# Kernel tuning notes

Hardware: AMD Instinct MI355X
Metric: run time of the kernel (lower is better)

The kernel has to match this reference:

```python
import jax, jax.numpy as jnp
import numpy as np

N_NODES = 50000
HEADS1 = 4
NEG_SLOPE = 0.2
EPS = 1e-16


def gat_conv(x, edge_index, W, att_src, att_dst, bias, heads, out_ch, concat):
    # edge_index: [2, E] with self-loops already appended by caller
    src, dst = edge_index[0], edge_index[1]
    N = x.shape[0]
    h = (x @ W).reshape(N, heads, out_ch)                      # [N, H, C]
    a_src = jnp.sum(h * att_src, axis=-1)                      # [N, H]
    a_dst = jnp.sum(h * att_dst, axis=-1)                      # [N, H]
    e = a_src[src] + a_dst[dst]                                # [E, H]
    e = jnp.where(e > 0, e, NEG_SLOPE * e)                     # leaky_relu
    m = jax.ops.segment_max(e, dst, num_segments=N)            # [N, H]
    alpha = jnp.exp(e - m[dst])                                # [E, H]
    denom = jax.ops.segment_sum(alpha, dst, num_segments=N)    # [N, H]
    alpha = alpha / (denom[dst] + EPS)                         # [E, H]
    msg = alpha[:, :, None] * h[src]                           # [E, H, C]
    out = jax.ops.segment_sum(msg, dst, num_segments=N)        # [N, H, C]
    if concat:
        out = out.reshape(N, heads * out_ch)
    else:
        out = out.mean(axis=1)
    return out + bias, alpha


def setup_inputs() -> dict:
    key = jax.random.key(0)
    ks = jax.random.split(key, 12)
    N, F, H, heads, C, E = N_NODES, 256, 64, HEADS1, 40, 800000
    g = 0.1
    return {
        "x": jax.random.normal(ks[0], (N, F), dtype=jnp.float32),
        "edge_index": jax.random.randint(ks[1], (2, E), 0, N, dtype=jnp.int32),
        "W1": jax.random.normal(ks[2], (F, heads * H), dtype=jnp.float32) * g,
        "att_src1": jax.random.normal(ks[3], (heads, H), dtype=jnp.float32) * g,
        "att_dst1": jax.random.normal(ks[4], (heads, H), dtype=jnp.float32) * g,
        "b1": jnp.zeros((heads * H,), dtype=jnp.float32),
        "W2": jax.random.normal(ks[5], (heads * H, C), dtype=jnp.float32) * g,
        "att_src2": jax.random.normal(ks[6], (1, C), dtype=jnp.float32) * g,
        "att_dst2": jax.random.normal(ks[7], (1, C), dtype=jnp.float32) * g,
        "b2": jnp.zeros((C,), dtype=jnp.float32),
    }


def reference(x, edge_index, W1, att_src1, att_dst1, b1, W2, att_src2, att_dst2, b2):
    N = x.shape[0]
    # add self-loops (PyG GATConv default)
    loops = jnp.arange(N, dtype=edge_index.dtype)
    ei = jnp.concatenate([edge_index, jnp.stack([loops, loops])], axis=1)
    # dropout is identity in eval mode
    h1, alpha = gat_conv(x, ei, W1, att_src1, att_dst1, b1,
                         HEADS1, W1.shape[1] // HEADS1, concat=True)
    h1 = jax.nn.elu(h1)
    h2, _ = gat_conv(h1, ei, W2, att_src2, att_dst2, b2,
                     1, W2.shape[1], concat=False)
    return jax.nn.log_softmax(h2, axis=1), alpha
```

## Files before the change

### kernel.cpp

```cpp
#include <hip/hip_runtime.h>
#include <math.h>

#define N_NODES 50000
#define HC1 256
#define H1 4
#define C2 40
#define C2P 64
#define E0 800000
#define ET 850000
#define NEG_SLOPE 0.2f
#define EPS_A 1e-16f

typedef __bf16 bf16x8 __attribute__((ext_vector_type(8)));
typedef float f32x4 __attribute__((ext_vector_type(4)));
typedef unsigned short u16x8 __attribute__((ext_vector_type(8)));


__device__ inline unsigned short f2bf(float f) {
    unsigned u = __float_as_uint(f);
    return (unsigned short)((u + 0x7FFFu + ((u >> 16) & 1u)) >> 16);
}
__device__ inline float bf_lo(unsigned q) { return __uint_as_float(q << 16); }
__device__ inline float bf_hi(unsigned q) { return __uint_as_float(q & 0xFFFF0000u); }


__device__ inline int edge_src(const int* __restrict__ ei, int e) {
    return (e < E0) ? ei[e] : (e - E0);
}
__device__ inline int edge_dst(const int* __restrict__ ei, int e) {
    return (e < E0) ? ei[E0 + e] : (e - E0);
}

__device__ inline void acc8(float ac[8], float A, uint4 q) {
    ac[0] += A * bf_lo(q.x); ac[1] += A * bf_hi(q.x);
    ac[2] += A * bf_lo(q.y); ac[3] += A * bf_hi(q.y);
    ac[4] += A * bf_lo(q.z); ac[5] += A * bf_hi(q.z);
    ac[6] += A * bf_lo(q.w); ac[7] += A * bf_hi(q.w);
}


#define CV_X 3200000
#define CV_W1 65536
#define CV_W2 16384
#define CV_TOT (CV_X + CV_W1 + CV_W2 + N_NODES)

__global__ void convert_all_kernel(const float* __restrict__ x,
                                   const float* __restrict__ W1,
                                   const float* __restrict__ W2,
                                   ushort4* __restrict__ xbf,
                                   unsigned short* __restrict__ w1t,
                                   unsigned short* __restrict__ w2t,
                                   int* __restrict__ deg) {
    int tid = blockIdx.x * blockDim.x + threadIdx.x;
    if (tid < CV_X) {
        float4 v = ((const float4*)x)[tid];
        ushort4 w;
        w.x = f2bf(v.x); w.y = f2bf(v.y); w.z = f2bf(v.z); w.w = f2bf(v.w);
        xbf[tid] = w;
    } else if (tid < CV_X + CV_W1) {
        int i = tid - CV_X;
        int n = i >> 8, k = i & 255;
        w1t[i] = f2bf(W1[k * 256 + n]);
    } else if (tid < CV_X + CV_W1 + CV_W2) {
        int i = tid - CV_X - CV_W1;
        int n = i >> 8, k = i & 255;
        w2t[i] = (n < C2) ? f2bf(W2[k * C2 + n]) : (unsigned short)0;
    } else if (tid < CV_TOT) {
        deg[tid - CV_X - CV_W1 - CV_W2] = 0;
    }
}


__global__ void hist_kernel(const int* __restrict__ ei, int* __restrict__ deg) {
    int e = blockIdx.x * blockDim.x + threadIdx.x;
    if (e >= ET) return;
    atomicAdd(&deg[edge_dst(ei, e)], 1);
}

__global__ __launch_bounds__(256) void scan_block_kernel(const int* __restrict__ deg,
                                                         int* __restrict__ excl,
                                                         int* __restrict__ bsum) {
    __shared__ int tmp[256];
    int t = threadIdx.x;
    int i = blockIdx.x * 256 + t;
    int v = (i < N_NODES) ? deg[i] : 0;
    tmp[t] = v;
    __syncthreads();
#pragma unroll
    for (int o = 1; o < 256; o <<= 1) {
        int x = (t >= o) ? tmp[t - o] : 0;
        __syncthreads();
        tmp[t] += x;
        __syncthreads();
    }
    if (i < N_NODES) excl[i] = tmp[t] - v;
    if (t == 255) bsum[blockIdx.x] = tmp[255];
}

#define NSCAN_B 196

__global__ __launch_bounds__(256) void scan_top_kernel(int* __restrict__ bsum) {
    __shared__ int tmp[256];
    int t = threadIdx.x;
    int v = (t < NSCAN_B) ? bsum[t] : 0;
    tmp[t] = v;
    __syncthreads();
#pragma unroll
    for (int o = 1; o < 256; o <<= 1) {
        int x = (t >= o) ? tmp[t - o] : 0;
        __syncthreads();
        tmp[t] += x;
        __syncthreads();
    }
    if (t < NSCAN_B) bsum[t] = tmp[t] - v;
}

__global__ __launch_bounds__(256) void scan_add_kernel(int* __restrict__ offsets,
                                                       int* __restrict__ cursor,
                                                       const int* __restrict__ bsum) {
    int i = blockIdx.x * 256 + threadIdx.x;
    if (i < N_NODES) {
        int v = offsets[i] + bsum[blockIdx.x];
        offsets[i] = v;
        cursor[i] = v;
    }
    if (i == 0) offsets[N_NODES] = ET;
}

__global__ void scatter_kernel(const int* __restrict__ ei, int* __restrict__ cursor,
                               int2* __restrict__ csr_es) {
    int e = blockIdx.x * blockDim.x + threadIdx.x;
    if (e >= ET) return;
    int d = edge_dst(ei, e);
    int pos = atomicAdd(&cursor[d], 1);
    csr_es[pos] = make_int2(e, edge_src(ei, e));
}


template <int TBM, int TBN, int WROWS, int WCOLS>
__global__ __launch_bounds__(256) void gemm_mfma_kernel(const unsigned short* __restrict__ Abf,
                                                        const unsigned short* __restrict__ Bt,
                                                        unsigned short* __restrict__ Cbf,
                                                        const float* __restrict__ att_s,
                                                        const float* __restrict__ att_d,
                                                        float* __restrict__ a_src_o,
                                                        float* __restrict__ a_dst_o,
                                                        int M, int Nc, int attN, int hstride) {
    static_assert(TBM == WROWS * 64 && TBN == WCOLS * 64, "tile");
    constexpr int LDK = 40;
    __shared__ alignas(16) unsigned short As[TBM * LDK];
    __shared__ alignas(16) unsigned short Bs[TBN * LDK];
    const int t = threadIdx.x;
    const int lane = t & 63;
    const int w = t >> 6;
    const int quad = lane >> 4;
    const int l16 = lane & 15;
    const int wm = (w / WCOLS) * 64;
    const int wn = (w % WCOLS) * 64;
    const int bm = blockIdx.x * TBM;
    const int bn = blockIdx.y * TBN;

    f32x4 acc[4][4] = {};

    for (int k0 = 0; k0 < 256; k0 += 32) {
        __syncthreads();
#pragma unroll
        for (int i = 0; i < TBM / 64; ++i) {
            int idx = t + i * 256;
            int row = idx >> 2, seg = idx & 3;
            u16x8 v = {};
            if (bm + row < M)
                v = *(const u16x8*)(Abf + (size_t)(bm + row) * 256 + k0 + seg * 8);
            *(u16x8*)&As[row * LDK + seg * 8] = v;
        }
#pragma unroll
        for (int i = 0; i < TBN / 64; ++i) {
            int idx = t + i * 256;
            int row = idx >> 2, seg = idx & 3;
            u16x8 v = *(const u16x8*)(Bt + (size_t)(bn + row) * 256 + k0 + seg * 8);
            *(u16x8*)&Bs[row * LDK + seg * 8] = v;
        }
        __syncthreads();

        bf16x8 af[4], bfr[4];
#pragma unroll
        for (int mi = 0; mi < 4; ++mi)
            af[mi] = *(const bf16x8*)&As[(wm + mi * 16 + l16) * LDK + quad * 8];
#pragma unroll
        for (int ni = 0; ni < 4; ++ni)
            bfr[ni] = *(const bf16x8*)&Bs[(wn + ni * 16 + l16) * LDK + quad * 8];
#pragma unroll
        for (int mi = 0; mi < 4; ++mi)
#pragma unroll
            for (int ni = 0; ni < 4; ++ni)
                acc[mi][ni] = __builtin_amdgcn_mfma_f32_16x16x32_bf16(
                    af[mi], bfr[ni], acc[mi][ni], 0, 0, 0);
    }

#pragma unroll
    for (int mi = 0; mi < 4; ++mi)
#pragma unroll
        for (int ni = 0; ni < 4; ++ni)
#pragma unroll
            for (int r = 0; r < 4; ++r) {
                int row = bm + wm + mi * 16 + quad * 4 + r;
                int col = bn + wn + ni * 16 + l16;
                if (row < M)
                    Cbf[(size_t)row * Nc + col] = f2bf(acc[mi][ni][r]);
            }

    float asc[4], adc[4];
#pragma unroll
    for (int ni = 0; ni < 4; ++ni) {
        int col = bn + wn + ni * 16 + l16;
        bool valid = col < attN;
        asc[ni] = valid ? att_s[col] : 0.f;
        adc[ni] = valid ? att_d[col] : 0.f;
    }
    float vs[16], vd[16];
#pragma unroll
    for (int mi = 0; mi < 4; ++mi)
#pragma unroll
        for (int r = 0; r < 4; ++r) {
            float s = 0.f, dd = 0.f;
#pragma unroll
            for (int ni = 0; ni < 4; ++ni) {
                s += acc[mi][ni][r] * asc[ni];
                dd += acc[mi][ni][r] * adc[ni];
            }
            vs[mi * 4 + r] = s;
            vd[mi * 4 + r] = dd;
        }
#pragma unroll
    for (int k = 0; k < 4; ++k) {
        const int o = 1 << k;
        const int b = (l16 >> k) & 1;
#pragma unroll
        for (int j = 0; j < (8 >> k); ++j) {
            float lo = vs[2 * j], hi = vs[2 * j + 1];
            float keep = b ? hi : lo, send = b ? lo : hi;
            vs[j] = keep + __shfl_xor(send, o);
            lo = vd[2 * j]; hi = vd[2 * j + 1];
            keep = b ? hi : lo; send = b ? lo : hi;
            vd[j] = keep + __shfl_xor(send, o);
        }
    }
    {
        int mi = l16 >> 2, r = l16 & 3;
        int row = bm + wm + mi * 16 + quad * 4 + r;
        int head = (bn + wn) >> 6;
        if (row < M) {
            a_src_o[(size_t)row * hstride + head] = vs[0];
            a_dst_o[(size_t)row * hstride + head] = vd[0];
        }
    }
}


__global__ __launch_bounds__(256) void l1_fused_kernel(const int* __restrict__ off,
                                                       const int2* __restrict__ csr_es,
                                                       const float4* __restrict__ a_src4,
                                                       const float4* __restrict__ a_dst4,
                                                       const unsigned* __restrict__ h1bf,
                                                       const float* __restrict__ b1,
                                                       float4* __restrict__ alpha_out4,
                                                       unsigned* __restrict__ out1bf) {
    __shared__ int    s_w[4][64];
    __shared__ float4 p_w[4][64];
    int t = threadIdx.x;
    int w = t >> 6, lane = t & 63;
    int d = blockIdx.x * 4 + w;
    int beg = off[d], end = off[d + 1];
    int deg = end - beg;
    int nch = (deg + 63) >> 6;
    int cnt0 = min(deg, 64);
    bool act0 = lane < cnt0;
    float4 ad4 = a_dst4[d];

    int2  es0 = make_int2(0, 0);
    float4 l0 = make_float4(-INFINITY, -INFINITY, -INFINITY, -INFINITY);
    float4 mx = l0;
    for (int cc = 0; cc < nch; ++cc) {
        int idx = beg + cc * 64 + lane;
        float4 l = make_float4(-INFINITY, -INFINITY, -INFINITY, -INFINITY);
        int2 es = make_int2(0, 0);
        if (idx < end) {
            es = csr_es[idx];
            float4 as4 = a_src4[es.y];
            l.x = as4.x + ad4.x; l.x = l.x > 0.f ? l.x : NEG_SLOPE * l.x;
            l.y = as4.y + ad4.y; l.y = l.y > 0.f ? l.y : NEG_SLOPE * l.y;
            l.z = as4.z + ad4.z; l.z = l.z > 0.f ? l.z : NEG_SLOPE * l.z;
            l.w = as4.w + ad4.w; l.w = l.w > 0.f ? l.w : NEG_SLOPE * l.w;
        }
        if (cc == 0) { es0 = es; l0 = l; }
        mx.x = fmaxf(mx.x, l.x); mx.y = fmaxf(mx.y, l.y);
        mx.z = fmaxf(mx.z, l.z); mx.w = fmaxf(mx.w, l.w);
    }
    int rdeg = cnt0;
    for (int o = 1; o < rdeg; o <<= 1) {
        mx.x = fmaxf(mx.x, __shfl_xor(mx.x, o));
        mx.y = fmaxf(mx.y, __shfl_xor(mx.y, o));
        mx.z = fmaxf(mx.z, __shfl_xor(mx.z, o));
        mx.w = fmaxf(mx.w, __shfl_xor(mx.w, o));
    }
    mx.x = __shfl(mx.x, 0); mx.y = __shfl(mx.y, 0);
    mx.z = __shfl(mx.z, 0); mx.w = __shfl(mx.w, 0);

    int hf = lane >> 5, li = lane & 31;
    int headc = li >> 3;
    float ac[8] = {};

    if (nch == 1) {
        float4 p0 = make_float4(0.f, 0.f, 0.f, 0.f);
        if (act0) {
            p0.x = __expf(l0.x - mx.x); p0.y = __expf(l0.y - mx.y);
            p0.z = __expf(l0.z - mx.z); p0.w = __expf(l0.w - mx.w);
            s_w[w][lane] = es0.y;
            p_w[w][lane] = p0;
        }
        const float* aw = (const float*)&p_w[w][0];
        int j = hf;
        for (; j + 6 < cnt0; j += 8) {
            int s0 = s_w[w][j],     s1 = s_w[w][j + 2];
            int s2 = s_w[w][j + 4], s3 = s_w[w][j + 6];
            float A0 = aw[4 * j + headc],       A1 = aw[4 * (j + 2) + headc];
            float A2 = aw[4 * (j + 4) + headc], A3 = aw[4 * (j + 6) + headc];
            uint4 q0 = *(const uint4*)&h1bf[(unsigned)s0 * 128u + 4u * li];
            uint4 q1 = *(const uint4*)&h1bf[(unsigned)s1 * 128u + 4u * li];
            uint4 q2 = *(const uint4*)&h1bf[(unsigned)s2 * 128u + 4u * li];
            uint4 q3 = *(const uint4*)&h1bf[(unsigned)s3 * 128u + 4u * li];
            acc8(ac, A0, q0); acc8(ac, A1, q1);
            acc8(ac, A2, q2); acc8(ac, A3, q3);
        }
        for (; j < cnt0; j += 2) {
            int s = s_w[w][j];
            float A = aw[4 * j + headc];
            uint4 q = *(const uint4*)&h1bf[(unsigned)s * 128u + 4u * li];
            acc8(ac, A, q);
        }

        float4 sum = p0;
        for (int o = 1; o < rdeg; o <<= 1) {
            sum.x += __shfl_xor(sum.x, o);
            sum.y += __shfl_xor(sum.y, o);
            sum.z += __shfl_xor(sum.z, o);
            sum.w += __shfl_xor(sum.w, o);
        }
        sum.x = __shfl(sum.x, 0); sum.y = __shfl(sum.y, 0);
        sum.z = __shfl(sum.z, 0); sum.w = __shfl(sum.w, 0);
        float4 inv;
        inv.x = 1.f / (sum.x + EPS_A); inv.y = 1.f / (sum.y + EPS_A);
        inv.z = 1.f / (sum.z + EPS_A); inv.w = 1.f / (sum.w + EPS_A);
        float invh = (headc == 0) ? inv.x : (headc == 1) ? inv.y
                   : (headc == 2) ? inv.z : inv.w;
#pragma unroll
        for (int c = 0; c < 8; ++c) ac[c] *= invh;
        if (act0) {
            float4 al0;
            al0.x = p0.x * inv.x; al0.y = p0.y * inv.y;
            al0.z = p0.z * inv.z; al0.w = p0.w * inv.w;
            alpha_out4[es0.x] = al0;
        }
    } else {
        float4 p0 = make_float4(0.f, 0.f, 0.f, 0.f);
        if (act0) {
            p0.x = __expf(l0.x - mx.x); p0.y = __expf(l0.y - mx.y);
            p0.z = __expf(l0.z - mx.z); p0.w = __expf(l0.w - mx.w);
        }
        float4 sum = p0;
        for (int cc = 1; cc < nch; ++cc) {
            int idx = beg + cc * 64 + lane;
            if (idx < end) {
                int2 es = csr_es[idx];
                float4 as4 = a_src4[es.y];
                float4 l;
                l.x = as4.x + ad4.x; l.x = l.x > 0.f ? l.x : NEG_SLOPE * l.x;
                l.y = as4.y + ad4.y; l.y = l.y > 0.f ? l.y : NEG_SLOPE * l.y;
                l.z = as4.z + ad4.z; l.z = l.z > 0.f ? l.z : NEG_SLOPE * l.z;
                l.w = as4.w + ad4.w; l.w = l.w > 0.f ? l.w : NEG_SLOPE * l.w;
                sum.x += __expf(l.x - mx.x); sum.y += __expf(l.y - mx.y);
                sum.z += __expf(l.z - mx.z); sum.w += __expf(l.w - mx.w);
            }
        }
        for (int o = 1; o < rdeg; o <<= 1) {
            sum.x += __shfl_xor(sum.x, o);
            sum.y += __shfl_xor(sum.y, o);
            sum.z += __shfl_xor(sum.z, o);
            sum.w += __shfl_xor(sum.w, o);
        }
        sum.x = __shfl(sum.x, 0); sum.y = __shfl(sum.y, 0);
        sum.z = __shfl(sum.z, 0); sum.w = __shfl(sum.w, 0);
        float4 inv;
        inv.x = 1.f / (sum.x + EPS_A); inv.y = 1.f / (sum.y + EPS_A);
        inv.z = 1.f / (sum.z + EPS_A); inv.w = 1.f / (sum.w + EPS_A);

        float4 al0;
        al0.x = p0.x * inv.x; al0.y = p0.y * inv.y;
        al0.z = p0.z * inv.z; al0.w = p0.w * inv.w;
        if (act0) {
            alpha_out4[es0.x] = al0;
            s_w[w][lane] = es0.y;
            p_w[w][lane] = al0;
        }
        const float* aw = (const float*)&p_w[w][0];
        int j = hf;
        for (; j + 2 < cnt0; j += 4) {
            int s0 = s_w[w][j], s1 = s_w[w][j + 2];
            float A0 = aw[4 * j + headc], A1 = aw[4 * (j + 2) + headc];
            uint4 q0 = *(const uint4*)&h1bf[(unsigned)s0 * 128u + 4u * li];
            uint4 q1 = *(const uint4*)&h1bf[(unsigned)s1 * 128u + 4u * li];
            acc8(ac, A0, q0); acc8(ac, A1, q1);
        }
        for (; j < cnt0; j += 2) {
            int s = s_w[w][j];
            float A = aw[4 * j + headc];
            uint4 q = *(const uint4*)&h1bf[(unsigned)s * 128u + 4u * li];
            acc8(ac, A, q);
        }
        for (int cc = 1; cc < nch; ++cc) {
            int idx = beg + cc * 64 + lane;
            int ms = 0;
            float4 ma = make_float4(0.f, 0.f, 0.f, 0.f);
            if (idx < end) {
                int2 es = csr_es[idx];
                ms = es.y;
                float4 as4 = a_src4[es.y];
                float4 l;
                l.x = as4.x + ad4.x; l.x = l.x > 0.f ? l.x : NEG_SLOPE * l.x;
                l.y = as4.y + ad4.y; l.y = l.y > 0.f ? l.y : NEG_SLOPE * l.y;
                l.z = as4.z + ad4.z; l.z = l.z > 0.f ? l.z : NEG_SLOPE * l.z;
                l.w = as4.w + ad4.w; l.w = l.w > 0.f ? l.w : NEG_SLOPE * l.w;
                ma.x = __expf(l.x - mx.x) * inv.x;
                ma.y = __expf(l.y - mx.y) * inv.y;
                ma.z = __expf(l.z - mx.z) * inv.z;
                ma.w = __expf(l.w - mx.w) * inv.w;
                alpha_out4[es.x] = ma;
            }
            int cnt = min(64, deg - cc * 64);
            for (int jj = hf; jj < cnt; jj += 2) {
                int s = __shfl(ms, jj);
                float h0 = __shfl(ma.x, jj), h1v = __shfl(ma.y, jj);
                float h2v = __shfl(ma.z, jj), h3 = __shfl(ma.w, jj);
                float A = (headc & 2) ? ((headc & 1) ? h3 : h2v) : ((headc & 1) ? h1v : h0);
                uint4 q = *(const uint4*)&h1bf[(unsigned)s * 128u + 4u * li];
                acc8(ac, A, q);
            }
        }
    }

#pragma unroll
    for (int c = 0; c < 8; ++c) ac[c] += __shfl_xor(ac[c], 32);
    if (hf == 0) {
        float4 bb0 = *(const float4*)&b1[8 * li];
        float4 bb1 = *(const float4*)&b1[8 * li + 4];
        float v0 = ac[0] + bb0.x, v1 = ac[1] + bb0.y;
        float v2 = ac[2] + bb0.z, v3 = ac[3] + bb0.w;
        float v4 = ac[4] + bb1.x, v5 = ac[5] + bb1.y;
        float v6 = ac[6] + bb1.z, v7 = ac[7] + bb1.w;
        v0 = v0 > 0.f ? v0 : __expf(v0) - 1.f;
        v1 = v1 > 0.f ? v1 : __expf(v1) - 1.f;
        v2 = v2 > 0.f ? v2 : __expf(v2) - 1.f;
        v3 = v3 > 0.f ? v3 : __expf(v3) - 1.f;
        v4 = v4 > 0.f ? v4 : __expf(v4) - 1.f;
        v5 = v5 > 0.f ? v5 : __expf(v5) - 1.f;
        v6 = v6 > 0.f ? v6 : __expf(v6) - 1.f;
        v7 = v7 > 0.f ? v7 : __expf(v7) - 1.f;
        uint4 qo;
        qo.x = ((unsigned)f2bf(v1) << 16) | (unsigned)f2bf(v0);
        qo.y = ((unsigned)f2bf(v3) << 16) | (unsigned)f2bf(v2);
        qo.z = ((unsigned)f2bf(v5) << 16) | (unsigned)f2bf(v4);
        qo.w = ((unsigned)f2bf(v7) << 16) | (unsigned)f2bf(v6);
        *(uint4*)&out1bf[(size_t)d * 128 + 4 * li] = qo;
    }
}


__global__ __launch_bounds__(256) void l2_fused_kernel(const int* __restrict__ off,
                                                       const int2* __restrict__ csr_es,
                                                       const float* __restrict__ a_src,
                                                       const float* __restrict__ a_dst,
                                                       const unsigned* __restrict__ h2bf,
                                                       const float* __restrict__ b2,
                                                       float* __restrict__ out) {
    __shared__ uint2 sp_w[4][64];
    int t = threadIdx.x;
    int w = t >> 6, lane = t & 63;
    int d = blockIdx.x * 4 + w;
    int beg = off[d], end = off[d + 1];
    int deg = end - beg;
    float ad = a_dst[d];
    int nch = (deg + 63) >> 6;
    int rdeg = min(deg, 64);

    int s0r = 0; float el0 = -INFINITY;
    float mx = -INFINITY;
    for (int cc = 0; cc < nch; ++cc) {
        int idx = beg + cc * 64 + lane;
        float el = -INFINITY; int s = 0;
        if (idx < end) {
            int2 es = csr_es[idx];
            s = es.y;
            el = a_src[s] + ad;
            el = el > 0.f ? el : NEG_SLOPE * el;
        }
        if (cc == 0) { el0 = el; s0r = s; }
        mx = fmaxf(mx, el);
    }
    for (int o = 1; o < rdeg; o <<= 1) mx = fmaxf(mx, __shfl_xor(mx, o));
    mx = __shfl(mx, 0);

    int hf = lane >> 5, li = lane & 31;
    float sum = 0.f, acc0 = 0.f, acc1 = 0.f;
    for (int cc = 0; cc < nch; ++cc) {
        int cnt = min(64, deg - cc * 64);
        float p = 0.f; int s = 0;
        if (cc == 0) {
            s = s0r;
            p = (lane < cnt) ? __expf(el0 - mx) : 0.f;
        } else {
            int idx = beg + cc * 64 + lane;
            if (idx < end) {
                int2 es = csr_es[idx];
                s = es.y;
                float el = a_src[s] + ad;
                el = el > 0.f ? el : NEG_SLOPE * el;
                p = __expf(el - mx);
            }
        }
        sum += p;
        if (lane < cnt) sp_w[w][lane] = make_uint2((unsigned)s, __float_as_uint(p));
        int j = hf;
        for (; j + 6 < cnt; j += 8) {
            uint2 e0 = sp_w[w][j],     e1 = sp_w[w][j + 2];
            uint2 e2 = sp_w[w][j + 4], e3 = sp_w[w][j + 6];
            float A0 = __uint_as_float(e0.y), A1 = __uint_as_float(e1.y);
            float A2 = __uint_as_float(e2.y), A3 = __uint_as_float(e3.y);
            unsigned q0 = h2bf[e0.x * 32u + li];
            unsigned q1 = h2bf[e1.x * 32u + li];
            unsigned q2 = h2bf[e2.x * 32u + li];
            unsigned q3 = h2bf[e3.x * 32u + li];
            acc0 += A0 * bf_lo(q0) + A1 * bf_lo(q1);
            acc1 += A0 * bf_hi(q0) + A1 * bf_hi(q1);
            acc0 += A2 * bf_lo(q2) + A3 * bf_lo(q3);
            acc1 += A2 * bf_hi(q2) + A3 * bf_hi(q3);
        }
        for (; j < cnt; j += 2) {
            uint2 e0 = sp_w[w][j];
            float A0 = __uint_as_float(e0.y);
            unsigned q = h2bf[e0.x * 32u + li];
            acc0 += A0 * bf_lo(q);
            acc1 += A0 * bf_hi(q);
        }
    }
    for (int o = 1; o < rdeg; o <<= 1) sum += __shfl_xor(sum, o);
    sum = __shfl(sum, 0);
    float inv = 1.f / (sum + EPS_A);

    acc0 += __shfl_xor(acc0, 32);
    acc1 += __shfl_xor(acc1, 32);
    acc0 *= inv;
    acc1 *= inv;
    bool act = li < 20;
    float v0 = act ? acc0 + b2[2 * li]     : -INFINITY;
    float v1 = act ? acc1 + b2[2 * li + 1] : -INFINITY;
    float mmx = fmaxf(v0, v1);
#pragma unroll
    for (int o = 16; o; o >>= 1) mmx = fmaxf(mmx, __shfl_xor(mmx, o));
    float ex = act ? __expf(v0 - mmx) + __expf(v1 - mmx) : 0.f;
#pragma unroll
    for (int o = 16; o; o >>= 1) ex += __shfl_xor(ex, o);
    float ls = __logf(ex);
    if (act && hf == 0)
        *(float2*)&out[(size_t)d * C2 + 2 * li] = make_float2(v0 - mmx - ls, v1 - mmx - ls);
}


extern "C" void kernel_launch(void* const* d_in, const int* in_sizes, int n_in,
                              void* d_out, int out_size, void* d_ws, size_t ws_size,
                              hipStream_t stream) {
    const float* x   = (const float*)d_in[0];
    const int*   ei  = (const int*)d_in[1];
    const float* W1  = (const float*)d_in[2];
    const float* as1 = (const float*)d_in[3];
    const float* ad1 = (const float*)d_in[4];
    const float* b1  = (const float*)d_in[5];
    const float* W2  = (const float*)d_in[6];
    const float* as2 = (const float*)d_in[7];
    const float* ad2 = (const float*)d_in[8];
    const float* b2  = (const float*)d_in[9];

    float* out   = (float*)d_out;
    float* alpha = out + (size_t)N_NODES * C2;

    unsigned* u32    = (unsigned*)d_ws;
    unsigned* h1bf   = u32;
    unsigned* xbf    = h1bf + 6400000;
    unsigned* h2bf   = xbf + 6400000;
    unsigned* w1t    = h2bf + 1600000;
    unsigned* w2t    = w1t + 32768;
    float* a_src1    = (float*)(w2t + 8192);
    float* a_dst1    = a_src1 + 200000;
    float* a_src2    = a_dst1 + 200000;
    float* a_dst2    = a_src2 + 50000;
    int*   deg       = (int*)(a_dst2 + 50000);
    int*   offs      = deg + 50000;
    int*   cursor    = offs + 50001;
    int*   bsum      = cursor + 50000;
    int2*  csr_es    = (int2*)(bsum + 257);
    unsigned* out1bf = xbf;

    const int TB = 256;
    const int EB = (ET + TB - 1) / TB;

    convert_all_kernel<<<(CV_TOT + TB - 1) / TB, TB, 0, stream>>>(
        x, W1, W2, (ushort4*)xbf, (unsigned short*)w1t, (unsigned short*)w2t, deg);

    hist_kernel<<<EB, TB, 0, stream>>>(ei, deg);
    scan_block_kernel<<<NSCAN_B, TB, 0, stream>>>(deg, offs, bsum);
    scan_top_kernel<<<1, TB, 0, stream>>>(bsum);
    scan_add_kernel<<<NSCAN_B, TB, 0, stream>>>(offs, cursor, bsum);
    scatter_kernel<<<EB, TB, 0, stream>>>(ei, cursor, csr_es);

    gemm_mfma_kernel<128, 128, 2, 2><<<dim3((N_NODES + 127) / 128, 2), TB, 0, stream>>>(
        (const unsigned short*)xbf, (const unsigned short*)w1t, (unsigned short*)h1bf,
        as1, ad1, a_src1, a_dst1, N_NODES, HC1, 256, H1);
    l1_fused_kernel<<<N_NODES / 4, TB, 0, stream>>>(offs, csr_es,
                                                    (const float4*)a_src1,
                                                    (const float4*)a_dst1,
                                                    h1bf, b1, (float4*)alpha, out1bf);

    gemm_mfma_kernel<256, 64, 4, 1><<<dim3((N_NODES + 255) / 256, 1), TB, 0, stream>>>(
        (const unsigned short*)out1bf, (const unsigned short*)w2t, (unsigned short*)h2bf,
        as2, ad2, a_src2, a_dst2, N_NODES, C2P, C2, 1);
    l2_fused_kernel<<<(N_NODES + 3) / 4, TB, 0, stream>>>(offs, csr_es, a_src2, a_dst2,
                                                          h2bf, b2, out);
}
```

Before: 362.3 us.

## Map one destination node per half-wavefront in both GAT aggregation kernels

The layer-1 and layer-2 aggregation kernels now give each 32-lane half of a wavefront its own destination node, so a block processes 8 nodes instead of 4. Each half gathers over all of its node's edges, which removes the cross-half shuffle reduction and the idle half-lanes when degree is small (about 17 on average). Softmax reductions now use a fixed 5-step butterfly, and the multi-chunk path is restructured into separate max, sum and accumulate passes. In exchange each lane serially gathers all neighbor rows, so per-node latency rises, and the extra passes recompute the logits.

```diff
diff --git a/kernel.cpp b/kernel.cpp
--- a/kernel.cpp
+++ b/kernel.cpp
@@ -37,6 +37,8 @@
     ac[4] += A * bf_lo(q.z); ac[5] += A * bf_hi(q.z);
     ac[6] += A * bf_lo(q.w); ac[7] += A * bf_hi(q.w);
 }
+
+__device__ inline float leaky(float v) { return v > 0.f ? v : NEG_SLOPE * v; }
 
 
 #define CV_X 3200000
@@ -265,66 +267,59 @@
                                                        const float* __restrict__ b1,
                                                        float4* __restrict__ alpha_out4,
                                                        unsigned* __restrict__ out1bf) {
-    __shared__ int    s_w[4][64];
-    __shared__ float4 p_w[4][64];
+    __shared__ int    s_w[4][2][32];
+    __shared__ float4 p_w[4][2][32];
     int t = threadIdx.x;
     int w = t >> 6, lane = t & 63;
-    int d = blockIdx.x * 4 + w;
+    int half = lane >> 5, li = lane & 31;
+    int d = blockIdx.x * 8 + w * 2 + half;
     int beg = off[d], end = off[d + 1];
     int deg = end - beg;
-    int nch = (deg + 63) >> 6;
-    int cnt0 = min(deg, 64);
-    bool act0 = lane < cnt0;
+    int nch = (deg + 31) >> 5;
+    int cnt0 = min(deg, 32);
+    bool act0 = li < cnt0;
     float4 ad4 = a_dst4[d];
-
-    int2  es0 = make_int2(0, 0);
-    float4 l0 = make_float4(-INFINITY, -INFINITY, -INFINITY, -INFINITY);
-    float4 mx = l0;
-    for (int cc = 0; cc < nch; ++cc) {
-        int idx = beg + cc * 64 + lane;
-        float4 l = make_float4(-INFINITY, -INFINITY, -INFINITY, -INFINITY);
-        int2 es = make_int2(0, 0);
-        if (idx < end) {
-            es = csr_es[idx];
-            float4 as4 = a_src4[es.y];
-            l.x = as4.x + ad4.x; l.x = l.x > 0.f ? l.x : NEG_SLOPE * l.x;
-            l.y = as4.y + ad4.y; l.y = l.y > 0.f ? l.y : NEG_SLOPE * l.y;
-            l.z = as4.z + ad4.z; l.z = l.z > 0.f ? l.z : NEG_SLOPE * l.z;
-            l.w = as4.w + ad4.w; l.w = l.w > 0.f ? l.w : NEG_SLOPE * l.w;
-        }
-        if (cc == 0) { es0 = es; l0 = l; }
-        mx.x = fmaxf(mx.x, l.x); mx.y = fmaxf(mx.y, l.y);
-        mx.z = fmaxf(mx.z, l.z); mx.w = fmaxf(mx.w, l.w);
-    }
-    int rdeg = cnt0;
-    for (int o = 1; o < rdeg; o <<= 1) {
-        mx.x = fmaxf(mx.x, __shfl_xor(mx.x, o));
-        mx.y = fmaxf(mx.y, __shfl_xor(mx.y, o));
-        mx.z = fmaxf(mx.z, __shfl_xor(mx.z, o));
-        mx.w = fmaxf(mx.w, __shfl_xor(mx.w, o));
-    }
-    mx.x = __shfl(mx.x, 0); mx.y = __shfl(mx.y, 0);
-    mx.z = __shfl(mx.z, 0); mx.w = __shfl(mx.w, 0);
-
-    int hf = lane >> 5, li = lane & 31;
     int headc = li >> 3;
+
     float ac[8] = {};
+    float4 sum = make_float4(0.f, 0.f, 0.f, 0.f);
+    float4 mx = make_float4(-INFINITY, -INFINITY, -INFINITY, -INFINITY);
+    int2 es0 = make_int2(0, 0);
+    float4 p0 = make_float4(0.f, 0.f, 0.f, 0.f);
+
+    const float* aw = (const float*)&p_w[w][half][0];
+    const int*   sw = &s_w[w][half][0];
 
     if (nch == 1) {
-        float4 p0 = make_float4(0.f, 0.f, 0.f, 0.f);
+        float4 l0 = make_float4(-INFINITY, -INFINITY, -INFINITY, -INFINITY);
         if (act0) {
-            p0.x = __expf(l0.x - mx.x); p0.y = __expf(l0.y - mx.y);
-            p0.z = __expf(l0.z - mx.z); p0.w = __expf(l0.w - mx.w);
-            s_w[w][lane] = es0.y;
-            p_w[w][lane] = p0;
-        }
-        const float* aw = (const float*)&p_w[w][0];
-        int j = hf;
-        for (; j + 6 < cnt0; j += 8) {
-            int s0 = s_w[w][j],     s1 = s_w[w][j + 2];
-            int s2 = s_w[w][j + 4], s3 = s_w[w][j + 6];
-            float A0 = aw[4 * j + headc],       A1 = aw[4 * (j + 2) + headc];
-            float A2 = aw[4 * (j + 4) + headc], A3 = aw[4 * (j + 6) + headc];
+            es0 = csr_es[beg + li];
+            float4 as4 = a_src4[es0.y];
+            l0.x = leaky(as4.x + ad4.x);
+            l0.y = leaky(as4.y + ad4.y);
+            l0.z = leaky(as4.z + ad4.z);
+            l0.w = leaky(as4.w + ad4.w);
+            s_w[w][half][li] = es0.y;
+        }
+        mx = l0;
+#pragma unroll
+        for (int o = 1; o <= 16; o <<= 1) {
+            mx.x = fmaxf(mx.x, __shfl_xor(mx.x, o));
+            mx.y = fmaxf(mx.y, __shfl_xor(mx.y, o));
+            mx.z = fmaxf(mx.z, __shfl_xor(mx.z, o));
+            mx.w = fmaxf(mx.w, __shfl_xor(mx.w, o));
+        }
+        p0.x = __expf(l0.x - mx.x);
+        p0.y = __expf(l0.y - mx.y);
+        p0.z = __expf(l0.z - mx.z);
+        p0.w = __expf(l0.w - mx.w);
+        if (act0) p_w[w][half][li] = p0;
+        sum = p0;
+        int j = 0;
+        for (; j + 3 < cnt0; j += 4) {
+            int s0 = sw[j], s1 = sw[j + 1], s2 = sw[j + 2], s3 = sw[j + 3];
+            float A0 = aw[4 * j + headc],       A1 = aw[4 * (j + 1) + headc];
+            float A2 = aw[4 * (j + 2) + headc], A3 = aw[4 * (j + 3) + headc];
             uint4 q0 = *(const uint4*)&h1bf[(unsigned)s0 * 128u + 4u * li];
             uint4 q1 = *(const uint4*)&h1bf[(unsigned)s1 * 128u + 4u * li];
             uint4 q2 = *(const uint4*)&h1bf[(unsigned)s2 * 128u + 4u * li];
@@ -332,29 +327,58 @@
             acc8(ac, A0, q0); acc8(ac, A1, q1);
             acc8(ac, A2, q2); acc8(ac, A3, q3);
         }
-        for (; j < cnt0; j += 2) {
-            int s = s_w[w][j];
+        for (; j < cnt0; ++j) {
+            int s = sw[j];
             float A = aw[4 * j + headc];
             uint4 q = *(const uint4*)&h1bf[(unsigned)s * 128u + 4u * li];
             acc8(ac, A, q);
         }
-
-        float4 sum = p0;
-        for (int o = 1; o < rdeg; o <<= 1) {
-            sum.x += __shfl_xor(sum.x, o);
-            sum.y += __shfl_xor(sum.y, o);
-            sum.z += __shfl_xor(sum.z, o);
-            sum.w += __shfl_xor(sum.w, o);
-        }
-        sum.x = __shfl(sum.x, 0); sum.y = __shfl(sum.y, 0);
-        sum.z = __shfl(sum.z, 0); sum.w = __shfl(sum.w, 0);
-        float4 inv;
-        inv.x = 1.f / (sum.x + EPS_A); inv.y = 1.f / (sum.y + EPS_A);
-        inv.z = 1.f / (sum.z + EPS_A); inv.w = 1.f / (sum.w + EPS_A);
-        float invh = (headc == 0) ? inv.x : (headc == 1) ? inv.y
-                   : (headc == 2) ? inv.z : inv.w;
-#pragma unroll
-        for (int c = 0; c < 8; ++c) ac[c] *= invh;
+    } else {
+        for (int cc = 0; cc < nch; ++cc) {
+            int idx = beg + cc * 32 + li;
+            if (idx < end) {
+                int2 es = csr_es[idx];
+                float4 as4 = a_src4[es.y];
+                mx.x = fmaxf(mx.x, leaky(as4.x + ad4.x));
+                mx.y = fmaxf(mx.y, leaky(as4.y + ad4.y));
+                mx.z = fmaxf(mx.z, leaky(as4.z + ad4.z));
+                mx.w = fmaxf(mx.w, leaky(as4.w + ad4.w));
+            }
+        }
+#pragma unroll
+        for (int o = 1; o <= 16; o <<= 1) {
+            mx.x = fmaxf(mx.x, __shfl_xor(mx.x, o));
+            mx.y = fmaxf(mx.y, __shfl_xor(mx.y, o));
+            mx.z = fmaxf(mx.z, __shfl_xor(mx.z, o));
+            mx.w = fmaxf(mx.w, __shfl_xor(mx.w, o));
+        }
+        for (int cc = 0; cc < nch; ++cc) {
+            int idx = beg + cc * 32 + li;
+            if (idx < end) {
+                int2 es = csr_es[idx];
+                float4 as4 = a_src4[es.y];
+                sum.x += __expf(leaky(as4.x + ad4.x) - mx.x);
+                sum.y += __expf(leaky(as4.y + ad4.y) - mx.y);
+                sum.z += __expf(leaky(as4.z + ad4.z) - mx.z);
+                sum.w += __expf(leaky(as4.w + ad4.w) - mx.w);
+            }
+        }
+    }
+
+#pragma unroll
+    for (int o = 1; o <= 16; o <<= 1) {
+        sum.x += __shfl_xor(sum.x, o);
+        sum.y += __shfl_xor(sum.y, o);
+        sum.z += __shfl_xor(sum.z, o);
+        sum.w += __shfl_xor(sum.w, o);
+    }
+    float4 inv;
+    inv.x = 1.f / (sum.x + EPS_A); inv.y = 1.f / (sum.y + EPS_A);
+    inv.z = 1.f / (sum.z + EPS_A); inv.w = 1.f / (sum.w + EPS_A);
+    float invh = (headc == 0) ? inv.x : (headc == 1) ? inv.y
+               : (headc == 2) ? inv.z : inv.w;
+
+    if (nch == 1) {
         if (act0) {
             float4 al0;
             al0.x = p0.x * inv.x; al0.y = p0.y * inv.y;
@@ -362,86 +386,27 @@
             alpha_out4[es0.x] = al0;
         }
     } else {
-        float4 p0 = make_float4(0.f, 0.f, 0.f, 0.f);
-        if (act0) {
-            p0.x = __expf(l0.x - mx.x); p0.y = __expf(l0.y - mx.y);
-            p0.z = __expf(l0.z - mx.z); p0.w = __expf(l0.w - mx.w);
-        }
-        float4 sum = p0;
-        for (int cc = 1; cc < nch; ++cc) {
-            int idx = beg + cc * 64 + lane;
+        for (int cc = 0; cc < nch; ++cc) {
+            int idx = beg + cc * 32 + li;
+            int cnt = min(32, deg - cc * 32);
             if (idx < end) {
                 int2 es = csr_es[idx];
                 float4 as4 = a_src4[es.y];
-                float4 l;
-                l.x = as4.x + ad4.x; l.x = l.x > 0.f ? l.x : NEG_SLOPE * l.x;
-                l.y = as4.y + ad4.y; l.y = l.y > 0.f ? l.y : NEG_SLOPE * l.y;
-                l.z = as4.z + ad4.z; l.z = l.z > 0.f ? l.z : NEG_SLOPE * l.z;
-                l.w = as4.w + ad4.w; l.w = l.w > 0.f ? l.w : NEG_SLOPE * l.w;
-                sum.x += __expf(l.x - mx.x); sum.y += __expf(l.y - mx.y);
-                sum.z += __expf(l.z - mx.z); sum.w += __expf(l.w - mx.w);
-            }
-        }
-        for (int o = 1; o < rdeg; o <<= 1) {
-            sum.x += __shfl_xor(sum.x, o);
-            sum.y += __shfl_xor(sum.y, o);
-            sum.z += __shfl_xor(sum.z, o);
-            sum.w += __shfl_xor(sum.w, o);
-        }
-        sum.x = __shfl(sum.x, 0); sum.y = __shfl(sum.y, 0);
-        sum.z = __shfl(sum.z, 0); sum.w = __shfl(sum.w, 0);
-        float4 inv;
-        inv.x = 1.f / (sum.x + EPS_A); inv.y = 1.f / (sum.y + EPS_A);
-        inv.z = 1.f / (sum.z + EPS_A); inv.w = 1.f / (sum.w + EPS_A);
-
-        float4 al0;
-        al0.x = p0.x * inv.x; al0.y = p0.y * inv.y;
-        al0.z = p0.z * inv.z; al0.w = p0.w * inv.w;
-        if (act0) {
-            alpha_out4[es0.x] = al0;
-            s_w[w][lane] = es0.y;
-            p_w[w][lane] = al0;
-        }
-        const float* aw = (const float*)&p_w[w][0];
-        int j = hf;
-        for (; j + 2 < cnt0; j += 4) {
-            int s0 = s_w[w][j], s1 = s_w[w][j + 2];
-            float A0 = aw[4 * j + headc], A1 = aw[4 * (j + 2) + headc];
-            uint4 q0 = *(const uint4*)&h1bf[(unsigned)s0 * 128u + 4u * li];
-            uint4 q1 = *(const uint4*)&h1bf[(unsigned)s1 * 128u + 4u * li];
-            acc8(ac, A0, q0); acc8(ac, A1, q1);
-        }
-        for (; j < cnt0; j += 2) {
-            int s = s_w[w][j];
-            float A = aw[4 * j + headc];
-            uint4 q = *(const uint4*)&h1bf[(unsigned)s * 128u + 4u * li];
-            acc8(ac, A, q);
-        }
-        for (int cc = 1; cc < nch; ++cc) {
-            int idx = beg + cc * 64 + lane;
-            int ms = 0;
-            float4 ma = make_float4(0.f, 0.f, 0.f, 0.f);
-            if (idx < end) {
-                int2 es = csr_es[idx];
-                ms = es.y;
-                float4 as4 = a_src4[es.y];
-                float4 l;
-                l.x = as4.x + ad4.x; l.x = l.x > 0.f ? l.x : NEG_SLOPE * l.x;
-                l.y = as4.y + ad4.y; l.y = l.y > 0.f ? l.y : NEG_SLOPE * l.y;
-                l.z = as4.z + ad4.z; l.z = l.z > 0.f ? l.z : NEG_SLOPE * l.z;
-                l.w = as4.w + ad4.w; l.w = l.w > 0.f ? l.w : NEG_SLOPE * l.w;
-                ma.x = __expf(l.x - mx.x) * inv.x;
-                ma.y = __expf(l.y - mx.y) * inv.y;
-                ma.z = __expf(l.z - mx.z) * inv.z;
-                ma.w = __expf(l.w - mx.w) * inv.w;
-                alpha_out4[es.x] = ma;
-            }
-            int cnt = min(64, deg - cc * 64);
-            for (int jj = hf; jj < cnt; jj += 2) {
-                int s = __shfl(ms, jj);
-                float h0 = __shfl(ma.x, jj), h1v = __shfl(ma.y, jj);
-                float h2v = __shfl(ma.z, jj), h3 = __shfl(ma.w, jj);
-                float A = (headc & 2) ? ((headc & 1) ? h3 : h2v) : ((headc & 1) ? h1v : h0);
+                float4 p;
+                p.x = __expf(leaky(as4.x + ad4.x) - mx.x);
+                p.y = __expf(leaky(as4.y + ad4.y) - mx.y);
+                p.z = __expf(leaky(as4.z + ad4.z) - mx.z);
+                p.w = __expf(leaky(as4.w + ad4.w) - mx.w);
+                float4 al;
+                al.x = p.x * inv.x; al.y = p.y * inv.y;
+                al.z = p.z * inv.z; al.w = p.w * inv.w;
+                alpha_out4[es.x] = al;
+                s_w[w][half][li] = es.y;
+                p_w[w][half][li] = p;
+            }
+            for (int j = 0; j < cnt; ++j) {
+                int s = sw[j];
+                float A = aw[4 * j + headc];
                 uint4 q = *(const uint4*)&h1bf[(unsigned)s * 128u + 4u * li];
                 acc8(ac, A, q);
             }
@@ -449,29 +414,28 @@
     }
 
 #pragma unroll
-    for (int c = 0; c < 8; ++c) ac[c] += __shfl_xor(ac[c], 32);
-    if (hf == 0) {
-        float4 bb0 = *(const float4*)&b1[8 * li];
-        float4 bb1 = *(const float4*)&b1[8 * li + 4];
-        float v0 = ac[0] + bb0.x, v1 = ac[1] + bb0.y;
-        float v2 = ac[2] + bb0.z, v3 = ac[3] + bb0.w;
-        float v4 = ac[4] + bb1.x, v5 = ac[5] + bb1.y;
-        float v6 = ac[6] + bb1.z, v7 = ac[7] + bb1.w;
-        v0 = v0 > 0.f ? v0 : __expf(v0) - 1.f;
-        v1 = v1 > 0.f ? v1 : __expf(v1) - 1.f;
-        v2 = v2 > 0.f ? v2 : __expf(v2) - 1.f;
-        v3 = v3 > 0.f ? v3 : __expf(v3) - 1.f;
-        v4 = v4 > 0.f ? v4 : __expf(v4) - 1.f;
-        v5 = v5 > 0.f ? v5 : __expf(v5) - 1.f;
-        v6 = v6 > 0.f ? v6 : __expf(v6) - 1.f;
-        v7 = v7 > 0.f ? v7 : __expf(v7) - 1.f;
-        uint4 qo;
-        qo.x = ((unsigned)f2bf(v1) << 16) | (unsigned)f2bf(v0);
-        qo.y = ((unsigned)f2bf(v3) << 16) | (unsigned)f2bf(v2);
-        qo.z = ((unsigned)f2bf(v5) << 16) | (unsigned)f2bf(v4);
-        qo.w = ((unsigned)f2bf(v7) << 16) | (unsigned)f2bf(v6);
-        *(uint4*)&out1bf[(size_t)d * 128 + 4 * li] = qo;
-    }
+    for (int c = 0; c < 8; ++c) ac[c] *= invh;
+
+    float4 bb0 = *(const float4*)&b1[8 * li];
+    float4 bb1 = *(const float4*)&b1[8 * li + 4];
+    float v0 = ac[0] + bb0.x, v1 = ac[1] + bb0.y;
+    float v2 = ac[2] + bb0.z, v3 = ac[3] + bb0.w;
+    float v4 = ac[4] + bb1.x, v5 = ac[5] + bb1.y;
+    float v6 = ac[6] + bb1.z, v7 = ac[7] + bb1.w;
+    v0 = v0 > 0.f ? v0 : __expf(v0) - 1.f;
+    v1 = v1 > 0.f ? v1 : __expf(v1) - 1.f;
+    v2 = v2 > 0.f ? v2 : __expf(v2) - 1.f;
+    v3 = v3 > 0.f ? v3 : __expf(v3) - 1.f;
+    v4 = v4 > 0.f ? v4 : __expf(v4) - 1.f;
+    v5 = v5 > 0.f ? v5 : __expf(v5) - 1.f;
+    v6 = v6 > 0.f ? v6 : __expf(v6) - 1.f;
+    v7 = v7 > 0.f ? v7 : __expf(v7) - 1.f;
+    uint4 qo;
+    qo.x = ((unsigned)f2bf(v1) << 16) | (unsigned)f2bf(v0);
+    qo.y = ((unsigned)f2bf(v3) << 16) | (unsigned)f2bf(v2);
+    qo.z = ((unsigned)f2bf(v5) << 16) | (unsigned)f2bf(v4);
+    qo.w = ((unsigned)f2bf(v7) << 16) | (unsigned)f2bf(v6);
+    *(uint4*)&out1bf[(size_t)d * 128 + 4 * li] = qo;
 }
 
 
@@ -482,57 +446,37 @@
                                                        const unsigned* __restrict__ h2bf,
                                                        const float* __restrict__ b2,
                                                        float* __restrict__ out) {
-    __shared__ uint2 sp_w[4][64];
+    __shared__ uint2 sp_w[4][2][32];
     int t = threadIdx.x;
     int w = t >> 6, lane = t & 63;
-    int d = blockIdx.x * 4 + w;
+    int half = lane >> 5, li = lane & 31;
+    int d = blockIdx.x * 8 + w * 2 + half;
     int beg = off[d], end = off[d + 1];
     int deg = end - beg;
     float ad = a_dst[d];
-    int nch = (deg + 63) >> 6;
-    int rdeg = min(deg, 64);
-
-    int s0r = 0; float el0 = -INFINITY;
-    float mx = -INFINITY;
-    for (int cc = 0; cc < nch; ++cc) {
-        int idx = beg + cc * 64 + lane;
-        float el = -INFINITY; int s = 0;
-        if (idx < end) {
-            int2 es = csr_es[idx];
-            s = es.y;
-            el = a_src[s] + ad;
-            el = el > 0.f ? el : NEG_SLOPE * el;
-        }
-        if (cc == 0) { el0 = el; s0r = s; }
-        mx = fmaxf(mx, el);
-    }
-    for (int o = 1; o < rdeg; o <<= 1) mx = fmaxf(mx, __shfl_xor(mx, o));
-    mx = __shfl(mx, 0);
-
-    int hf = lane >> 5, li = lane & 31;
+    int nch = (deg + 31) >> 5;
+    int cnt0 = min(deg, 32);
+    bool act0 = li < cnt0;
+
     float sum = 0.f, acc0 = 0.f, acc1 = 0.f;
-    for (int cc = 0; cc < nch; ++cc) {
-        int cnt = min(64, deg - cc * 64);
-        float p = 0.f; int s = 0;
-        if (cc == 0) {
-            s = s0r;
-            p = (lane < cnt) ? __expf(el0 - mx) : 0.f;
-        } else {
-            int idx = beg + cc * 64 + lane;
-            if (idx < end) {
-                int2 es = csr_es[idx];
-                s = es.y;
-                float el = a_src[s] + ad;
-                el = el > 0.f ? el : NEG_SLOPE * el;
-                p = __expf(el - mx);
-            }
-        }
-        sum += p;
-        if (lane < cnt) sp_w[w][lane] = make_uint2((unsigned)s, __float_as_uint(p));
-        int j = hf;
-        for (; j + 6 < cnt; j += 8) {
-            uint2 e0 = sp_w[w][j],     e1 = sp_w[w][j + 2];
-            uint2 e2 = sp_w[w][j + 4], e3 = sp_w[w][j + 6];
+
+    if (nch == 1) {
+        float el0 = -INFINITY; int s0 = 0;
+        if (act0) {
+            int2 es = csr_es[beg + li];
+            s0 = es.y;
+            el0 = leaky(a_src[s0] + ad);
+        }
+        float mx = el0;
+#pragma unroll
+        for (int o = 1; o <= 16; o <<= 1) mx = fmaxf(mx, __shfl_xor(mx, o));
+        float p0 = __expf(el0 - mx);
+        if (act0) sp_w[w][half][li] = make_uint2((unsigned)s0, __float_as_uint(p0));
+        sum = p0;
+        int j = 0;
+        for (; j + 3 < cnt0; j += 4) {
+            uint2 e0 = sp_w[w][half][j],     e1 = sp_w[w][half][j + 1];
+            uint2 e2 = sp_w[w][half][j + 2], e3 = sp_w[w][half][j + 3];
             float A0 = __uint_as_float(e0.y), A1 = __uint_as_float(e1.y);
             float A2 = __uint_as_float(e2.y), A3 = __uint_as_float(e3.y);
             unsigned q0 = h2bf[e0.x * 32u + li];
@@ -544,22 +488,50 @@
             acc0 += A2 * bf_lo(q2) + A3 * bf_lo(q3);
             acc1 += A2 * bf_hi(q2) + A3 * bf_hi(q3);
         }
-        for (; j < cnt; j += 2) {
-            uint2 e0 = sp_w[w][j];
+        for (; j < cnt0; ++j) {
+            uint2 e0 = sp_w[w][half][j];
             float A0 = __uint_as_float(e0.y);
             unsigned q = h2bf[e0.x * 32u + li];
             acc0 += A0 * bf_lo(q);
             acc1 += A0 * bf_hi(q);
         }
-    }
-    for (int o = 1; o < rdeg; o <<= 1) sum += __shfl_xor(sum, o);
-    sum = __shfl(sum, 0);
+    } else {
+        float mx = -INFINITY;
+        for (int cc = 0; cc < nch; ++cc) {
+            int idx = beg + cc * 32 + li;
+            if (idx < end) {
+                int2 es = csr_es[idx];
+                mx = fmaxf(mx, leaky(a_src[es.y] + ad));
+            }
+        }
+#pragma unroll
+        for (int o = 1; o <= 16; o <<= 1) mx = fmaxf(mx, __shfl_xor(mx, o));
+        for (int cc = 0; cc < nch; ++cc) {
+            int idx = beg + cc * 32 + li;
+            int cnt = min(32, deg - cc * 32);
+            if (idx < end) {
+                int2 es = csr_es[idx];
+                float el = leaky(a_src[es.y] + ad);
+                float p = __expf(el - mx);
+                sum += p;
+                sp_w[w][half][li] = make_uint2((unsigned)es.y, __float_as_uint(p));
+            }
+            for (int j = 0; j < cnt; ++j) {
+                uint2 e0 = sp_w[w][half][j];
+                float A0 = __uint_as_float(e0.y);
+                unsigned q = h2bf[e0.x * 32u + li];
+                acc0 += A0 * bf_lo(q);
+                acc1 += A0 * bf_hi(q);
+            }
+        }
+    }
+
+#pragma unroll
+    for (int o = 1; o <= 16; o <<= 1) sum += __shfl_xor(sum, o);
     float inv = 1.f / (sum + EPS_A);
-
-    acc0 += __shfl_xor(acc0, 32);
-    acc1 += __shfl_xor(acc1, 32);
     acc0 *= inv;
     acc1 *= inv;
+
     bool act = li < 20;
     float v0 = act ? acc0 + b2[2 * li]     : -INFINITY;
     float v1 = act ? acc1 + b2[2 * li + 1] : -INFINITY;
@@ -570,7 +542,7 @@
 #pragma unroll
     for (int o = 16; o; o >>= 1) ex += __shfl_xor(ex, o);
     float ls = __logf(ex);
-    if (act && hf == 0)
+    if (act)
         *(float2*)&out[(size_t)d * C2 + 2 * li] = make_float2(v0 - mmx - ls, v1 - mmx - ls);
 }
 
@@ -624,7 +596,7 @@
     gemm_mfma_kernel<128, 128, 2, 2><<<dim3((N_NODES + 127) / 128, 2), TB, 0, stream>>>(
         (const unsigned short*)xbf, (const unsigned short*)w1t, (unsigned short*)h1bf,
         as1, ad1, a_src1, a_dst1, N_NODES, HC1, 256, H1);
-    l1_fused_kernel<<<N_NODES / 4, TB, 0, stream>>>(offs, csr_es,
+    l1_fused_kernel<<<N_NODES / 8, TB, 0, stream>>>(offs, csr_es,
                                                     (const float4*)a_src1,
                                                     (const float4*)a_dst1,
                                                     h1bf, b1, (float4*)alpha, out1bf);
@@ -632,6 +604,6 @@
     gemm_mfma_kernel<256, 64, 4, 1><<<dim3((N_NODES + 255) / 256, 1), TB, 0, stream>>>(
         (const unsigned short*)out1bf, (const unsigned short*)w2t, (unsigned short*)h2bf,
         as2, ad2, a_src2, a_dst2, N_NODES, C2P, C2, 1);
-    l2_fused_kernel<<<(N_NODES + 3) / 4, TB, 0, stream>>>(offs, csr_es, a_src2, a_dst2,
-                                                          h2bf, b2, out);
-}
+    l2_fused_kernel<<<N_NODES / 8, TB, 0, stream>>>(offs, csr_es, a_src2, a_dst2,
+                                                    h2bf, b2, out);
+}
```

Result: faster. 354.7 us (-2.1%).
